# Optimization experiments

Measured on AMD Instinct MI355X. Metric: run time of the kernel, lower is better.

Reference implementation:

```python
import jax, jax.numpy as jnp
import numpy as np

N = 50000
E = 800000
H_IN = 64
HEADS1 = 4
NEG_SLOPE = 0.2


def gat_conv(x, W, att_src, att_dst, bias, src, dst, heads, out_ch):
    """PyG GATConv (add_self_loops=False, concat=True).
    x: [N, in]; W: [in, heads*out_ch]; att_*: [heads, out_ch]; bias: [heads*out_ch].
    """
    n = x.shape[0]
    h = (x @ W).reshape(n, heads, out_ch)                 # [N, H, C]
    a_s = jnp.einsum('nhc,hc->nh', h, att_src)            # [N, H]
    a_d = jnp.einsum('nhc,hc->nh', h, att_dst)            # [N, H]
    e = jax.nn.leaky_relu(a_s[src] + a_d[dst], NEG_SLOPE) # [E, H]
    # segment softmax over incoming edges of each destination node
    e_max = jax.ops.segment_max(e, dst, num_segments=n)
    e_exp = jnp.exp(e - e_max[dst])
    denom = jax.ops.segment_sum(e_exp, dst, num_segments=n)
    alpha = e_exp / denom[dst]                            # [E, H]
    msg = h[src] * alpha[:, :, None]                      # [E, H, C]
    out = jax.ops.segment_sum(msg, dst, num_segments=n)   # [N, H, C]
    return out.reshape(n, heads * out_ch) + bias


def setup_inputs() -> dict:
    key = jax.random.key(0)
    ks = jax.random.split(key, 10)
    x = jax.random.normal(ks[0], (N, H_IN), dtype=jnp.float32)
    edge_index = jax.random.randint(ks[1], (2, E), 0, N, dtype=jnp.int64)
    s1 = 1.0 / np.sqrt(H_IN)
    W1 = jax.random.normal(ks[2], (H_IN, HEADS1 * H_IN), dtype=jnp.float32) * s1
    att_src1 = jax.random.normal(ks[3], (HEADS1, H_IN), dtype=jnp.float32) * s1
    att_dst1 = jax.random.normal(ks[4], (HEADS1, H_IN), dtype=jnp.float32) * s1
    b1 = jnp.zeros((HEADS1 * H_IN,), dtype=jnp.float32)
    s2 = 1.0 / np.sqrt(HEADS1 * H_IN)
    W2 = jax.random.normal(ks[5], (HEADS1 * H_IN, H_IN), dtype=jnp.float32) * s2
    att_src2 = jax.random.normal(ks[6], (1, H_IN), dtype=jnp.float32) * s2
    att_dst2 = jax.random.normal(ks[7], (1, H_IN), dtype=jnp.float32) * s2
    b2 = jnp.zeros((H_IN,), dtype=jnp.float32)
    return {"x": x, "edge_index": edge_index, "W1": W1, "att_src1": att_src1,
            "att_dst1": att_dst1, "b1": b1, "W2": W2, "att_src2": att_src2,
            "att_dst2": att_dst2, "b2": b2}


def reference(x, edge_index, W1, att_src1, att_dst1, b1, W2, att_src2, att_dst2, b2):
    src, dst = edge_index[0], edge_index[1]
    h = gat_conv(x, W1, att_src1, att_dst1, b1, src, dst, HEADS1, H_IN)
    h = jax.nn.relu(h)
    out = gat_conv(h, W2, att_src2, att_dst2, b2, src, dst, 1, H_IN)
    return out
```

## Files before the change

### kernel.cpp

```cpp
#include <hip/hip_runtime.h>
#include <hip/hip_fp16.h>

#define NEG_SLOPE 0.2f
#define H_IN 64

typedef _Float16 h2vec __attribute__((ext_vector_type(2)));

__device__ __forceinline__ float lrelu(float v) { return v > 0.f ? v : NEG_SLOPE * v; }

__device__ __forceinline__ void cvt4(uint2 g, float* o) {
    __half2 lo = *(__half2*)&g.x, hi = *(__half2*)&g.y;
    float2 a = __half22float2(lo), b = __half22float2(hi);
    o[0] = a.x; o[1] = a.y; o[2] = b.x; o[3] = b.y;
}

__device__ __forceinline__ float fdot2h(float xf, h2vec w, float acc) {
#if __has_builtin(__builtin_amdgcn_fdot2)
    union { float f; h2vec h; } cv; cv.f = xf;
    return __builtin_amdgcn_fdot2(cv.h, w, acc, false);
#else
    union { float f; __half2 h; } cv; cv.f = xf;
    float2 g = __half22float2(cv.h);
    acc = fmaf(g.x, (float)w[0], acc);
    return fmaf(g.y, (float)w[1], acc);
#endif
}

__global__ __launch_bounds__(256) void zero_micro(
    int* __restrict__ deg, int* __restrict__ cursor, int n,
    const float* __restrict__ W1, const float* __restrict__ as1, const float* __restrict__ ad1,
    const float* __restrict__ W2, const float* __restrict__ as2, const float* __restrict__ ad2,
    float* __restrict__ wa1s, float* __restrict__ wa1d,
    float* __restrict__ wa2s, float* __restrict__ wa2d)
{
    int tid = threadIdx.x;
    if (blockIdx.x > 0) {
        int i = (blockIdx.x - 1) * 256 + tid;
        if (i < n) { deg[i] = 0; cursor[i] = 0; }
        return;
    }
    int k = tid >> 2, h = tid & 3;
    float s = 0.f, d = 0.f;
    #pragma unroll 8
    for (int c = 0; c < 64; ++c) {
        float w = W1[k * 256 + h * 64 + c];
        s = fmaf(w, as1[h * 64 + c], s);
        d = fmaf(w, ad1[h * 64 + c], d);
    }
    wa1s[k * 4 + h] = s; wa1d[k * 4 + h] = d;
    float s2 = 0.f, d2 = 0.f;
    #pragma unroll 8
    for (int c = 0; c < 64; ++c) {
        float w = W2[tid * 64 + c];
        s2 = fmaf(w, as2[c], s2);
        d2 = fmaf(w, ad2[c], d2);
    }
    wa2s[tid] = s2; wa2d[tid] = d2;
}

__global__ __launch_bounds__(256) void hist_kernel(const int* __restrict__ dst,
                                                   int* __restrict__ deg, int ne)
{
    int e = blockIdx.x * 256 + threadIdx.x;
    if (e < ne) atomicAdd(&deg[dst[e]], 1);
}

__global__ __launch_bounds__(256) void block_sum(const int* __restrict__ deg,
                                                 int* __restrict__ bsum, int n)
{
    __shared__ int part[4];
    int i = blockIdx.x * 256 + threadIdx.x;
    int v = (i < n) ? deg[i] : 0;
    #pragma unroll
    for (int off = 32; off; off >>= 1) v += __shfl_down(v, off);
    int lane = threadIdx.x & 63, wv = threadIdx.x >> 6;
    if (lane == 0) part[wv] = v;
    __syncthreads();
    if (threadIdx.x == 0)
        bsum[blockIdx.x] = part[0] + part[1] + part[2] + part[3];
}

__global__ __launch_bounds__(256) void scan_bsum(const int* __restrict__ bsum,
                                                 int* __restrict__ bpre, int nb)
{
    __shared__ int sm[256];
    int t = threadIdx.x;
    int v = (t < nb) ? bsum[t] : 0;
    sm[t] = v; __syncthreads();
    for (int off = 1; off < 256; off <<= 1) {
        int y = (t >= off) ? sm[t - off] : 0;
        __syncthreads();
        if (t >= off) sm[t] += y;
        __syncthreads();
    }
    if (t < nb) bpre[t] = sm[t] - v;
}

__global__ __launch_bounds__(256) void scan_rowptr(const int* __restrict__ deg,
                                                   const int* __restrict__ bpre,
                                                   int* __restrict__ rowptr, int n)
{
    __shared__ int sm[256];
    int t = threadIdx.x;
    int i = blockIdx.x * 256 + t;
    int v = (i < n) ? deg[i] : 0;
    sm[t] = v; __syncthreads();
    for (int off = 1; off < 256; off <<= 1) {
        int y = (t >= off) ? sm[t - off] : 0;
        __syncthreads();
        if (t >= off) sm[t] += y;
        __syncthreads();
    }
    if (i < n) rowptr[i] = sm[t] - v + bpre[blockIdx.x];
}

__global__ __launch_bounds__(256) void scatter_kernel(
    const int* __restrict__ src, const int* __restrict__ dst,
    const int* __restrict__ rowptr, int* __restrict__ cursor,
    int* __restrict__ csr_src, int ne)
{
    int e = blockIdx.x * 256 + threadIdx.x;
    if (e >= ne) return;
    int t = dst[e];
    int pos = atomicAdd(&cursor[t], 1);
    csr_src[rowptr[t] + pos] = src[e];
}

__global__ __launch_bounds__(256) void axw1_kernel(
    const float* __restrict__ x,
    const float* __restrict__ wa1s, const float* __restrict__ wa1d,
    float* __restrict__ a_s, float* __restrict__ a_d, int n)
{
    __shared__ float ws[256], wd[256];
    int tid = threadIdx.x;
    ws[tid] = wa1s[tid]; wd[tid] = wa1d[tid];
    __syncthreads();
    int row = blockIdx.x * 256 + tid;
    if (row >= n) return;
    const float4* xv = (const float4*)(x + (size_t)row * 64);
    float aS[4] = {0, 0, 0, 0}, aD[4] = {0, 0, 0, 0};
    #pragma unroll
    for (int k4 = 0; k4 < 16; ++k4) {
        float4 q = xv[k4];
        float xe[4] = {q.x, q.y, q.z, q.w};
        #pragma unroll
        for (int e = 0; e < 4; ++e) {
            int k = k4 * 4 + e;
            #pragma unroll
            for (int h = 0; h < 4; ++h) {
                aS[h] = fmaf(xe[e], ws[k * 4 + h], aS[h]);
                aD[h] = fmaf(xe[e], wd[k * 4 + h], aD[h]);
            }
        }
    }
    #pragma unroll
    for (int h = 0; h < 4; ++h) {
        a_s[row * 4 + h] = aS[h];
        a_d[row * 4 + h] = aD[h];
    }
}

__global__ __launch_bounds__(256) void gemm1_kernel(
    const float* __restrict__ x, const float* __restrict__ W1,
    __half* __restrict__ h1, int n)
{
    __shared__ float w_s[32 * 256];
    int tid = threadIdx.x;
    int row0 = blockIdx.x * 16;
    float acc[16];
    #pragma unroll
    for (int r = 0; r < 16; ++r) acc[r] = 0.f;

    const float4* Wv = (const float4*)W1;
    for (int kk = 0; kk < 2; ++kk) {
        if (kk) __syncthreads();
        {
            float4* wv = (float4*)w_s;
            #pragma unroll
            for (int i = 0; i < 8; ++i)
                wv[tid + i * 256] = Wv[kk * 2048 + tid + i * 256];
        }
        __syncthreads();
        #pragma unroll 2
        for (int k4 = 0; k4 < 8; ++k4) {
            float4 q[16];
            #pragma unroll
            for (int r = 0; r < 16; ++r)
                q[r] = *(const float4*)(x + (size_t)(row0 + r) * 64 + kk * 32 + k4 * 4);
            #pragma unroll
            for (int e = 0; e < 4; ++e) {
                float w = w_s[(k4 * 4 + e) * 256 + tid];
                #pragma unroll
                for (int r = 0; r < 16; ++r)
                    acc[r] = fmaf(((const float*)&q[r])[e], w, acc[r]);
            }
        }
    }
    #pragma unroll
    for (int r = 0; r < 16; ++r)
        h1[(size_t)(row0 + r) * 256 + tid] = __float2half(acc[r]);
}

__global__ __launch_bounds__(256) void gemm2_kernel(
    const __half* __restrict__ xr, const float* __restrict__ W2,
    __half* __restrict__ h2, int n)
{
    __shared__ h2vec w_s[128 * 64];
    int tid = threadIdx.x;
    #pragma unroll 4
    for (int i = 0; i < 32; ++i) {
        int idx = tid + i * 256;
        int kp = idx >> 6, col = idx & 63;
        h2vec v;
        v[0] = (_Float16)W2[(2 * kp) * 64 + col];
        v[1] = (_Float16)W2[(2 * kp + 1) * 64 + col];
        w_s[idx] = v;
    }
    __syncthreads();
    int col = tid & 63, wv_ = tid >> 6;
    int row0 = blockIdx.x * 64 + wv_ * 16;
    float acc[16];
    #pragma unroll
    for (int r = 0; r < 16; ++r) acc[r] = 0.f;

    const float4* xb = (const float4*)(xr + (size_t)row0 * 256);
    for (int g = 0; g < 32; ++g) {
        float4 q[16];
        #pragma unroll
        for (int r = 0; r < 16; ++r) q[r] = xb[r * 32 + g];
        #pragma unroll
        for (int e = 0; e < 4; ++e) {
            h2vec w = w_s[(g * 4 + e) * 64 + col];
            #pragma unroll
            for (int r = 0; r < 16; ++r)
                acc[r] = fdot2h(((const float*)&q[r])[e], w, acc[r]);
        }
    }
    #pragma unroll
    for (int r = 0; r < 16; ++r) {
        int row = row0 + r;
        if (row < n) h2[(size_t)row * 64 + col] = __float2half(acc[r]);
    }
}

__global__ __launch_bounds__(256) void aggr1_csr(
    const int* __restrict__ rowptr, const int* __restrict__ deg,
    const int* __restrict__ csr_src,
    const float* __restrict__ a_s, const float* __restrict__ a_d,
    const __half* __restrict__ h1, const float* __restrict__ b1,
    const float* __restrict__ wa2s, const float* __restrict__ wa2d,
    __half* __restrict__ out1r, float* __restrict__ a_s2, float* __restrict__ a_d2,
    int n)
{
    __shared__ float al[4][64];
    __shared__ int   ss[64];
    __shared__ float ev[4][128];
    __shared__ float pm[3][64][4];
    int t = blockIdx.x;
    int tid = threadIdx.x, h = tid >> 6, lane = tid & 63;
    int row0 = rowptr[t], d = deg[t];
    float adt = a_d[t * 4 + h];
    bool small = (d <= 128);

    float m = -INFINITY;
    if (small) {
        for (int i = lane; i < d; i += 64) {
            float v = lrelu(a_s[csr_src[row0 + i] * 4 + h] + adt);
            ev[h][i] = v;
            m = fmaxf(m, v);
        }
    } else {
        for (int i = lane; i < d; i += 64)
            m = fmaxf(m, lrelu(a_s[csr_src[row0 + i] * 4 + h] + adt));
    }
    #pragma unroll
    for (int off = 32; off; off >>= 1) m = fmaxf(m, __shfl_xor(m, off));

    float dsum = 0.f;
    if (small) {
        for (int i = lane; i < d; i += 64) {
            float e = __expf(ev[h][i] - m);
            ev[h][i] = e;
            dsum += e;
        }
    } else {
        for (int i = lane; i < d; i += 64)
            dsum += __expf(lrelu(a_s[csr_src[row0 + i] * 4 + h] + adt) - m);
    }
    #pragma unroll
    for (int off = 32; off; off >>= 1) dsum += __shfl_xor(dsum, off);
    float inv = (d > 0) ? 1.f / dsum : 0.f;

    int c4 = tid & 63;
    int p = tid >> 6;
    int hc = c4 >> 4;
    float acc[4] = {0.f, 0.f, 0.f, 0.f};
    const uint2* hb = (const uint2*)h1;

    for (int c0 = 0; c0 < d; c0 += 64) {
        int i = c0 + lane;
        float alpha = 0.f;
        if (i < d) {
            if (small) alpha = ev[h][i] * inv;
            else alpha = __expf(lrelu(a_s[csr_src[row0 + i] * 4 + h] + adt) - m) * inv;
        }
        al[h][lane] = alpha;
        if (h == 0) ss[lane] = (i < d) ? csr_src[row0 + i] * 64 : 0;
        __syncthreads();
        int cl = min(64, d - c0);
        int j = p;
        for (; j + 4 < cl; j += 8) {
            float a0 = al[hc][j], a1 = al[hc][j + 4];
            uint2 g0 = hb[ss[j] + c4];
            uint2 g1 = hb[ss[j + 4] + c4];
            float f0[4], f1[4];
            cvt4(g0, f0); cvt4(g1, f1);
            #pragma unroll
            for (int q = 0; q < 4; ++q) {
                acc[q] = fmaf(a0, f0[q], acc[q]);
                acc[q] = fmaf(a1, f1[q], acc[q]);
            }
        }
        if (j < cl) {
            float a0 = al[hc][j];
            uint2 g0 = hb[ss[j] + c4];
            float f0[4];
            cvt4(g0, f0);
            #pragma unroll
            for (int q = 0; q < 4; ++q) acc[q] = fmaf(a0, f0[q], acc[q]);
        }
        __syncthreads();
    }

    if (p) {
        #pragma unroll
        for (int q = 0; q < 4; ++q) pm[p - 1][c4][q] = acc[q];
    }
    __syncthreads();
    if (p == 0) {
        float4 bb = ((const float4*)b1)[c4];
        float r0 = fmaxf(acc[0] + pm[0][c4][0] + pm[1][c4][0] + pm[2][c4][0] + bb.x, 0.f);
        float r1 = fmaxf(acc[1] + pm[0][c4][1] + pm[1][c4][1] + pm[2][c4][1] + bb.y, 0.f);
        float r2 = fmaxf(acc[2] + pm[0][c4][2] + pm[1][c4][2] + pm[2][c4][2] + bb.z, 0.f);
        float r3 = fmaxf(acc[3] + pm[0][c4][3] + pm[1][c4][3] + pm[2][c4][3] + bb.w, 0.f);
        __half2 lo = __floats2half2_rn(r0, r1), hi = __floats2half2_rn(r2, r3);
        uint2 o; o.x = *(unsigned*)&lo; o.y = *(unsigned*)&hi;
        ((uint2*)out1r)[(size_t)t * 64 + c4] = o;
        float4 ws4 = ((const float4*)wa2s)[c4];
        float4 wd4 = ((const float4*)wa2d)[c4];
        float s2  = r0 * ws4.x + r1 * ws4.y + r2 * ws4.z + r3 * ws4.w;
        float d2v = r0 * wd4.x + r1 * wd4.y + r2 * wd4.z + r3 * wd4.w;
        #pragma unroll
        for (int off = 32; off; off >>= 1) {
            s2  += __shfl_down(s2, off);
            d2v += __shfl_down(d2v, off);
        }
        if (tid == 0) { a_s2[t] = s2; a_d2[t] = d2v; }
    }
}

__global__ __launch_bounds__(256) void aggr2_csr(
    const int* __restrict__ rowptr, const int* __restrict__ deg,
    const int* __restrict__ csr_src,
    const float* __restrict__ a_s, const float* __restrict__ a_d,
    const __half* __restrict__ h2, const float* __restrict__ b2,
    float* __restrict__ dout, int n)
{
    __shared__ float ev2[4][128];
    __shared__ float al2[4][64];
    __shared__ int   ss2[4][64];
    int wv = threadIdx.x >> 6, lane = threadIdx.x & 63;
    int t = blockIdx.x * 4 + wv;
    if (t >= n) return;
    int row0 = rowptr[t], d = deg[t];
    float adt = a_d[t];
    bool small = (d <= 128);

    float m = -INFINITY;
    if (small) {
        for (int i = lane; i < d; i += 64) {
            float v = lrelu(a_s[csr_src[row0 + i]] + adt);
            ev2[wv][i] = v;
            m = fmaxf(m, v);
        }
    } else {
        for (int i = lane; i < d; i += 64)
            m = fmaxf(m, lrelu(a_s[csr_src[row0 + i]] + adt));
    }
    #pragma unroll
    for (int off = 32; off; off >>= 1) m = fmaxf(m, __shfl_xor(m, off));

    float dsum = 0.f;
    if (small) {
        for (int i = lane; i < d; i += 64) {
            float e = __expf(ev2[wv][i] - m);
            ev2[wv][i] = e;
            dsum += e;
        }
    } else {
        for (int i = lane; i < d; i += 64)
            dsum += __expf(lrelu(a_s[csr_src[row0 + i]] + adt) - m);
    }
    #pragma unroll
    for (int off = 32; off; off >>= 1) dsum += __shfl_xor(dsum, off);
    float inv = (d > 0) ? 1.f / dsum : 0.f;

    int c4 = lane & 15;
    int p = lane >> 4;
    float acc[4] = {0.f, 0.f, 0.f, 0.f};
    const uint2* hb = (const uint2*)h2;

    for (int c0 = 0; c0 < d; c0 += 64) {
        int i = c0 + lane;
        float alpha = 0.f; int so = 0;
        if (i < d) {
            int s = csr_src[row0 + i];
            so = s * 16;
            if (small) alpha = ev2[wv][i] * inv;
            else alpha = __expf(lrelu(a_s[s] + adt) - m) * inv;
        }
        al2[wv][lane] = alpha;
        ss2[wv][lane] = so;
        int cl = min(64, d - c0);
        int j = p;
        for (; j + 4 < cl; j += 8) {
            float a0 = al2[wv][j], a1 = al2[wv][j + 4];
            uint2 g0 = hb[ss2[wv][j] + c4];
            uint2 g1 = hb[ss2[wv][j + 4] + c4];
            float f0[4], f1[4];
            cvt4(g0, f0); cvt4(g1, f1);
            #pragma unroll
            for (int q = 0; q < 4; ++q) {
                acc[q] = fmaf(a0, f0[q], acc[q]);
                acc[q] = fmaf(a1, f1[q], acc[q]);
            }
        }
        if (j < cl) {
            float a0 = al2[wv][j];
            uint2 g0 = hb[ss2[wv][j] + c4];
            float f0[4];
            cvt4(g0, f0);
            #pragma unroll
            for (int q = 0; q < 4; ++q) acc[q] = fmaf(a0, f0[q], acc[q]);
        }
    }

    #pragma unroll
    for (int q = 0; q < 4; ++q) {
        acc[q] += __shfl_down(acc[q], 32);
        acc[q] += __shfl_down(acc[q], 16);
    }
    if (p == 0) {
        float4 bb = ((const float4*)b2)[c4];
        float4 o;
        o.x = acc[0] + bb.x; o.y = acc[1] + bb.y;
        o.z = acc[2] + bb.z; o.w = acc[3] + bb.w;
        ((float4*)(dout + (size_t)t * 64))[c4] = o;
    }
}

extern "C" void kernel_launch(void* const* d_in, const int* in_sizes, int n_in,
                              void* d_out, int out_size, void* d_ws, size_t ws_size,
                              hipStream_t stream)
{
    const float* x    = (const float*)d_in[0];
    const int*   ei   = (const int*)d_in[1];
    const float* W1   = (const float*)d_in[2];
    const float* as1  = (const float*)d_in[3];
    const float* ad1  = (const float*)d_in[4];
    const float* b1   = (const float*)d_in[5];
    const float* W2   = (const float*)d_in[6];
    const float* as2  = (const float*)d_in[7];
    const float* ad2  = (const float*)d_in[8];
    const float* b2   = (const float*)d_in[9];
    float* dout = (float*)d_out;

    const int n  = in_sizes[0] / H_IN;
    const int ne = in_sizes[1] / 2;
    const int* src = ei;
    const int* dst = ei + ne;
    const int NB = (n + 255) / 256;

    float* ws = (float*)d_ws;
    __half* h1h   = (__half*)ws;
    __half* out1r = h1h + (size_t)n * 256;
    float* fbase  = ws + (size_t)n * 256;
    float* a_s1   = fbase;
    float* a_d1   = a_s1   + (size_t)n * 4;
    float* a_s2   = a_d1   + (size_t)n * 4;
    float* a_d2   = a_s2   + (size_t)n;
    float* wa1s   = a_d2   + (size_t)n;
    float* wa1d   = wa1s + 256;
    float* wa2s   = wa1d + 256;
    float* wa2d   = wa2s + 256;
    int*   deg    = (int*)(wa2d + 256);
    int*   rowptr = deg + n;
    int*   csr    = rowptr + n;
    int*   bsum   = csr + ne;
    int*   bpre   = bsum + NB;
    int*   cursor = (int*)h1h;
    __half* h2h   = h1h;

    zero_micro<<<NB + 1, 256, 0, stream>>>(deg, cursor, n, W1, as1, ad1,
                                           W2, as2, ad2, wa1s, wa1d, wa2s, wa2d);

    hist_kernel<<<(ne + 255) / 256, 256, 0, stream>>>(dst, deg, ne);
    block_sum<<<NB, 256, 0, stream>>>(deg, bsum, n);
    scan_bsum<<<1, 256, 0, stream>>>(bsum, bpre, NB);
    scan_rowptr<<<NB, 256, 0, stream>>>(deg, bpre, rowptr, n);
    scatter_kernel<<<(ne + 255) / 256, 256, 0, stream>>>(src, dst, rowptr, cursor, csr, ne);

    axw1_kernel<<<NB, 256, 0, stream>>>(x, wa1s, wa1d, a_s1, a_d1, n);
    gemm1_kernel<<<n / 16, 256, 0, stream>>>(x, W1, h1h, n);
    aggr1_csr<<<n, 256, 0, stream>>>(rowptr, deg, csr, a_s1, a_d1, h1h, b1,
                                     wa2s, wa2d, out1r, a_s2, a_d2, n);

    gemm2_kernel<<<(n + 63) / 64, 256, 0, stream>>>(out1r, W2, h2h, n);
    aggr2_csr<<<(n + 3) / 4, 256, 0, stream>>>(rowptr, deg, csr, a_s2, a_d2, h2h, b2, dout, n);
}
```

Baseline: 426.3 us.

## Use online softmax in aggregation, seed cursor with rowptr, vectorize hist/scatter

Both aggregation kernels now compute the segment max and sum in one pass using an online-softmax merge, including across the wave, instead of two separate passes with two reductions. The exponent is recomputed when alpha is formed. The CSR scatter cursor is now initialized to rowptr inside the scan kernel, which drops the separate zeroing and the rowptr load in scatter. The histogram and scatter kernels each handle two edges per thread with int2 loads. Shared-memory arrays are padded to reduce bank conflicts. In exchange, each edge does extra exp work in the online update, and the grid sizing for an odd edge count uses ne/2, which could drop the last edge.

Result: slower. 435.5 us (+2.2%).

```diff
diff --git a/kernel.cpp b/kernel.cpp
--- a/kernel.cpp
+++ b/kernel.cpp
@@ -26,8 +26,20 @@
 #endif
 }
 
+#define NEG_BIG -1e30f
+
+__device__ __forceinline__ void wave_online(float& lm, float& ls) {
+    #pragma unroll
+    for (int off = 32; off; off >>= 1) {
+        float om = __shfl_xor(lm, off), os = __shfl_xor(ls, off);
+        float M = fmaxf(lm, om);
+        ls = ls * __expf(lm - M) + os * __expf(om - M);
+        lm = M;
+    }
+}
+
 __global__ __launch_bounds__(256) void zero_micro(
-    int* __restrict__ deg, int* __restrict__ cursor, int n,
+    int* __restrict__ deg, int n,
     const float* __restrict__ W1, const float* __restrict__ as1, const float* __restrict__ ad1,
     const float* __restrict__ W2, const float* __restrict__ as2, const float* __restrict__ ad2,
     float* __restrict__ wa1s, float* __restrict__ wa1d,
@@ -36,7 +48,7 @@
     int tid = threadIdx.x;
     if (blockIdx.x > 0) {
         int i = (blockIdx.x - 1) * 256 + tid;
-        if (i < n) { deg[i] = 0; cursor[i] = 0; }
+        if (i < n) deg[i] = 0;
         return;
     }
     int k = tid >> 2, h = tid & 3;
@@ -61,8 +73,14 @@
 __global__ __launch_bounds__(256) void hist_kernel(const int* __restrict__ dst,
                                                    int* __restrict__ deg, int ne)
 {
-    int e = blockIdx.x * 256 + threadIdx.x;
-    if (e < ne) atomicAdd(&deg[dst[e]], 1);
+    int e = (blockIdx.x * 256 + threadIdx.x) * 2;
+    if (e + 1 < ne) {
+        int2 dd = *(const int2*)(dst + e);
+        atomicAdd(&deg[dd.x], 1);
+        atomicAdd(&deg[dd.y], 1);
+    } else if (e < ne) {
+        atomicAdd(&deg[dst[e]], 1);
+    }
 }
 
 __global__ __launch_bounds__(256) void block_sum(const int* __restrict__ deg,
@@ -98,7 +116,8 @@
 
 __global__ __launch_bounds__(256) void scan_rowptr(const int* __restrict__ deg,
                                                    const int* __restrict__ bpre,
-                                                   int* __restrict__ rowptr, int n)
+                                                   int* __restrict__ rowptr,
+                                                   int* __restrict__ cursor, int n)
 {
     __shared__ int sm[256];
     int t = threadIdx.x;
@@ -111,19 +130,26 @@
         if (t >= off) sm[t] += y;
         __syncthreads();
     }
-    if (i < n) rowptr[i] = sm[t] - v + bpre[blockIdx.x];
+    if (i < n) {
+        int rp = sm[t] - v + bpre[blockIdx.x];
+        rowptr[i] = rp;
+        cursor[i] = rp;
+    }
 }
 
 __global__ __launch_bounds__(256) void scatter_kernel(
     const int* __restrict__ src, const int* __restrict__ dst,
-    const int* __restrict__ rowptr, int* __restrict__ cursor,
-    int* __restrict__ csr_src, int ne)
-{
-    int e = blockIdx.x * 256 + threadIdx.x;
-    if (e >= ne) return;
-    int t = dst[e];
-    int pos = atomicAdd(&cursor[t], 1);
-    csr_src[rowptr[t] + pos] = src[e];
+    int* __restrict__ cursor, int* __restrict__ csr_src, int ne)
+{
+    int e = (blockIdx.x * 256 + threadIdx.x) * 2;
+    if (e + 1 < ne) {
+        int2 sv = *(const int2*)(src + e);
+        int2 dv = *(const int2*)(dst + e);
+        csr_src[atomicAdd(&cursor[dv.x], 1)] = sv.x;
+        csr_src[atomicAdd(&cursor[dv.y], 1)] = sv.y;
+    } else if (e < ne) {
+        csr_src[atomicAdd(&cursor[dst[e]], 1)] = src[e];
+    }
 }
 
 __global__ __launch_bounds__(256) void axw1_kernel(
@@ -252,44 +278,35 @@
     __half* __restrict__ out1r, float* __restrict__ a_s2, float* __restrict__ a_d2,
     int n)
 {
-    __shared__ float al[4][64];
+    __shared__ float al[4][68];
     __shared__ int   ss[64];
     __shared__ float ev[4][128];
-    __shared__ float pm[3][64][4];
+    __shared__ float pm[3][64][5];
     int t = blockIdx.x;
     int tid = threadIdx.x, h = tid >> 6, lane = tid & 63;
     int row0 = rowptr[t], d = deg[t];
     float adt = a_d[t * 4 + h];
     bool small = (d <= 128);
 
-    float m = -INFINITY;
+    float lm = NEG_BIG, ls = 0.f;
     if (small) {
         for (int i = lane; i < d; i += 64) {
             float v = lrelu(a_s[csr_src[row0 + i] * 4 + h] + adt);
             ev[h][i] = v;
-            m = fmaxf(m, v);
+            float M = fmaxf(lm, v);
+            ls = ls * __expf(lm - M) + __expf(v - M);
+            lm = M;
         }
     } else {
-        for (int i = lane; i < d; i += 64)
-            m = fmaxf(m, lrelu(a_s[csr_src[row0 + i] * 4 + h] + adt));
-    }
-    #pragma unroll
-    for (int off = 32; off; off >>= 1) m = fmaxf(m, __shfl_xor(m, off));
-
-    float dsum = 0.f;
-    if (small) {
         for (int i = lane; i < d; i += 64) {
-            float e = __expf(ev[h][i] - m);
-            ev[h][i] = e;
-            dsum += e;
-        }
-    } else {
-        for (int i = lane; i < d; i += 64)
-            dsum += __expf(lrelu(a_s[csr_src[row0 + i] * 4 + h] + adt) - m);
-    }
-    #pragma unroll
-    for (int off = 32; off; off >>= 1) dsum += __shfl_xor(dsum, off);
-    float inv = (d > 0) ? 1.f / dsum : 0.f;
+            float v = lrelu(a_s[csr_src[row0 + i] * 4 + h] + adt);
+            float M = fmaxf(lm, v);
+            ls = ls * __expf(lm - M) + __expf(v - M);
+            lm = M;
+        }
+    }
+    wave_online(lm, ls);
+    float inv = (d > 0) ? 1.f / ls : 0.f;
 
     int c4 = tid & 63;
     int p = tid >> 6;
@@ -301,8 +318,8 @@
         int i = c0 + lane;
         float alpha = 0.f;
         if (i < d) {
-            if (small) alpha = ev[h][i] * inv;
-            else alpha = __expf(lrelu(a_s[csr_src[row0 + i] * 4 + h] + adt) - m) * inv;
+            float v = small ? ev[h][i] : lrelu(a_s[csr_src[row0 + i] * 4 + h] + adt);
+            alpha = __expf(v - lm) * inv;
         }
         al[h][lane] = alpha;
         if (h == 0) ss[lane] = (i < d) ? csr_src[row0 + i] * 64 : 0;
@@ -376,34 +393,25 @@
     float adt = a_d[t];
     bool small = (d <= 128);
 
-    float m = -INFINITY;
+    float lm = NEG_BIG, ls = 0.f;
     if (small) {
         for (int i = lane; i < d; i += 64) {
             float v = lrelu(a_s[csr_src[row0 + i]] + adt);
             ev2[wv][i] = v;
-            m = fmaxf(m, v);
+            float M = fmaxf(lm, v);
+            ls = ls * __expf(lm - M) + __expf(v - M);
+            lm = M;
         }
     } else {
-        for (int i = lane; i < d; i += 64)
-            m = fmaxf(m, lrelu(a_s[csr_src[row0 + i]] + adt));
-    }
-    #pragma unroll
-    for (int off = 32; off; off >>= 1) m = fmaxf(m, __shfl_xor(m, off));
-
-    float dsum = 0.f;
-    if (small) {
         for (int i = lane; i < d; i += 64) {
-            float e = __expf(ev2[wv][i] - m);
-            ev2[wv][i] = e;
-            dsum += e;
-        }
-    } else {
-        for (int i = lane; i < d; i += 64)
-            dsum += __expf(lrelu(a_s[csr_src[row0 + i]] + adt) - m);
-    }
-    #pragma unroll
-    for (int off = 32; off; off >>= 1) dsum += __shfl_xor(dsum, off);
-    float inv = (d > 0) ? 1.f / dsum : 0.f;
+            float v = lrelu(a_s[csr_src[row0 + i]] + adt);
+            float M = fmaxf(lm, v);
+            ls = ls * __expf(lm - M) + __expf(v - M);
+            lm = M;
+        }
+    }
+    wave_online(lm, ls);
+    float inv = (d > 0) ? 1.f / ls : 0.f;
 
     int c4 = lane & 15;
     int p = lane >> 4;
@@ -416,8 +424,8 @@
         if (i < d) {
             int s = csr_src[row0 + i];
             so = s * 16;
-            if (small) alpha = ev2[wv][i] * inv;
-            else alpha = __expf(lrelu(a_s[s] + adt) - m) * inv;
+            float v = small ? ev2[wv][i] : lrelu(a_s[s] + adt);
+            alpha = __expf(v - lm) * inv;
         }
         al2[wv][lane] = alpha;
         ss2[wv][lane] = so;
@@ -501,14 +509,14 @@
     int*   cursor = (int*)h1h;
     __half* h2h   = h1h;
 
-    zero_micro<<<NB + 1, 256, 0, stream>>>(deg, cursor, n, W1, as1, ad1,
+    zero_micro<<<NB + 1, 256, 0, stream>>>(deg, n, W1, as1, ad1,
                                            W2, as2, ad2, wa1s, wa1d, wa2s, wa2d);
 
-    hist_kernel<<<(ne + 255) / 256, 256, 0, stream>>>(dst, deg, ne);
+    hist_kernel<<<(ne / 2 + 255) / 256, 256, 0, stream>>>(dst, deg, ne);
     block_sum<<<NB, 256, 0, stream>>>(deg, bsum, n);
     scan_bsum<<<1, 256, 0, stream>>>(bsum, bpre, NB);
-    scan_rowptr<<<NB, 256, 0, stream>>>(deg, bpre, rowptr, n);
-    scatter_kernel<<<(ne + 255) / 256, 256, 0, stream>>>(src, dst, rowptr, cursor, csr, ne);
+    scan_rowptr<<<NB, 256, 0, stream>>>(deg, bpre, rowptr, cursor, n);
+    scatter_kernel<<<(ne / 2 + 255) / 256, 256, 0, stream>>>(src, dst, cursor, csr, ne);
 
     axw1_kernel<<<NB, 256, 0, stream>>>(x, wa1s, wa1d, a_s1, a_d1, n);
     gemm1_kernel<<<n / 16, 256, 0, stream>>>(x, W1, h1h, n);
```
